# Performance work log

Measured on AMD Instinct MI355X. Metric: run time of the kernel, lower is better.

The kernel has to match this reference:

```python
import jax, jax.numpy as jnp
import numpy as np

WIN = 8          # window size
P = 32           # patch grid side (patch_w_num)
SHIFTS = (0, 4)  # stride=[0,4] -> regular + shifted window branches
HEADS = 16
DH = 64          # dim_head
DIM = 512
HP = HEADS // len(SHIFTS)   # heads per shift branch
NW = (P // WIN) ** 2        # windows per image (16)
WS = WIN * WIN              # tokens per window (64)


def _rel_index():
    c = np.stack(np.meshgrid(np.arange(WIN), np.arange(WIN), indexing="ij")).reshape(2, -1)
    r = (c[:, :, None] - c[:, None, :]).transpose(1, 2, 0) + WIN - 1
    return (r[..., 0] * (2 * WIN - 1) + r[..., 1]).astype(np.int32)  # [WS, WS]

REL_IDX = _rel_index()


def _shift_mask(shift):
    # standard Swin attention mask for cyclic shift
    img = np.zeros((P, P), np.int32); cnt = 0
    sl = (slice(0, -WIN), slice(-WIN, -shift), slice(-shift, None))
    for hs in sl:
        for ws_ in sl:
            img[hs, ws_] = cnt; cnt += 1
    m = img.reshape(P // WIN, WIN, P // WIN, WIN).transpose(0, 2, 1, 3).reshape(NW, WS)
    return np.where(m[:, None, :] != m[:, :, None], -1e9, 0.0).astype(np.float32)  # [NW, WS, WS]

MASK4 = _shift_mask(4)


def _part(t):
    # [B,P,P,hp,dh] -> [B*NW, hp, WS, dh]
    B, _, _, hp, dh = t.shape
    t = t.reshape(B, P // WIN, WIN, P // WIN, WIN, hp, dh)
    t = t.transpose(0, 1, 3, 2, 4, 5, 6).reshape(B * NW, WS, hp, dh)
    return t.transpose(0, 2, 1, 3)


def _merge(t, B):
    # [B*NW, hp, WS, dh] -> [B,P,P,hp,dh]
    hp, dh = t.shape[1], t.shape[3]
    t = t.transpose(0, 2, 1, 3).reshape(B, P // WIN, P // WIN, WIN, WIN, hp, dh)
    return t.transpose(0, 1, 3, 2, 4, 5, 6).reshape(B, P, P, hp, dh)


def setup_inputs() -> dict:
    key = jax.random.key(0)
    ks = jax.random.split(key, 5)
    B = 64
    x = jax.random.normal(ks[0], (B, P * P, DIM), jnp.float32)
    w_qkv = jax.random.normal(ks[1], (DIM, 3 * HEADS * DH), jnp.float32) * (DIM ** -0.5)
    bias_table = jax.random.normal(ks[2], ((2 * WIN - 1) ** 2, HEADS), jnp.float32) * 0.02
    w_out = jax.random.normal(ks[3], (HEADS * DH, DIM), jnp.float32) * ((HEADS * DH) ** -0.5)
    b_out = jnp.zeros((DIM,), jnp.float32)
    return {"x": x, "w_qkv": w_qkv, "bias_table": bias_table, "w_out": w_out, "b_out": b_out}


def reference(x, w_qkv, bias_table, w_out, b_out):
    B, N, _ = x.shape
    scale = DH ** -0.5
    qkv = (x @ w_qkv).reshape(B, P, P, 3, HEADS, DH)
    q, k, v = qkv[..., 0, :, :], qkv[..., 1, :, :], qkv[..., 2, :, :]  # [B,P,P,HEADS,DH]
    bias = bias_table[REL_IDX].transpose(2, 0, 1)  # [HEADS, WS, WS]
    mask4 = jnp.asarray(MASK4)
    outs = []
    for i, shift in enumerate(SHIFTS):
        hs = slice(i * HP, (i + 1) * HP)
        qi, ki, vi = q[..., hs, :], k[..., hs, :], v[..., hs, :]
        if shift:
            qi = jnp.roll(qi, (-shift, -shift), axis=(1, 2))
            ki = jnp.roll(ki, (-shift, -shift), axis=(1, 2))
            vi = jnp.roll(vi, (-shift, -shift), axis=(1, 2))
        qw, kw, vw = _part(qi), _part(ki), _part(vi)  # [B*NW, HP, WS, DH]
        attn = jnp.einsum("whid,whjd->whij", qw * scale, kw) + bias[hs][None]
        if shift:
            attn = attn.reshape(B, NW, HP, WS, WS) + mask4[None, :, None]
            attn = attn.reshape(B * NW, HP, WS, WS)
        attn = jax.nn.softmax(attn, axis=-1)
        ow = jnp.einsum("whij,whjd->whid", attn, vw)
        oi = _merge(ow, B)
        if shift:
            oi = jnp.roll(oi, (shift, shift), axis=(1, 2))
        outs.append(oi)
    out = jnp.concatenate(outs, axis=3).reshape(B, N, HEADS * DH)
    return out @ w_out + b_out
```

## Files before the change

### kernel.cpp

```cpp
#include <hip/hip_runtime.h>
#include <hip/hip_bf16.h>


typedef __attribute__((ext_vector_type(4))) float f32x4;
typedef __attribute__((ext_vector_type(8))) __bf16 bf16x8;
typedef __attribute__((ext_vector_type(8))) unsigned short u16x8;

__device__ __forceinline__ unsigned short f2bf(float f) {
  __hip_bfloat16 h = __float2bfloat16(f);
  return __builtin_bit_cast(unsigned short, h);
}
__device__ __forceinline__ float bf2f(unsigned short u) {
  return __builtin_bit_cast(float, ((unsigned int)u) << 16);
}

#define GLL16(gsrc, ldst)                                                              \
  __builtin_amdgcn_global_load_lds((const __attribute__((address_space(1))) void*)(gsrc), \
                                   (__attribute__((address_space(3))) void*)(ldst), 16, 0, 0)

#define SWZ(x) ((x) ^ ((((x) >> 7) & 3) << 4))

#define MFMA_BF16 __builtin_amdgcn_mfma_f32_16x16x32_bf16

__global__ __launch_bounds__(256) void cvt_x_kernel(const float* __restrict__ in,
                                                    unsigned short* __restrict__ out, int n4) {
  int i = blockIdx.x * blockDim.x + threadIdx.x;
  int stride = gridDim.x * blockDim.x;
  for (; i < n4; i += stride) {
    float4 v = reinterpret_cast<const float4*>(in)[i];
    ushort4 o;
    o.x = f2bf(v.x); o.y = f2bf(v.y); o.z = f2bf(v.z); o.w = f2bf(v.w);
    reinterpret_cast<ushort4*>(out)[i] = o;
  }
}

__global__ __launch_bounds__(256) void cvt_T_kernel(const float* __restrict__ in,
                                                    unsigned short* __restrict__ out,
                                                    int R, int C) {
  int idx = blockIdx.x * 256 + threadIdx.x;
  if (idx < R * C) {
    int r = idx / C, c = idx - r * C;
    out[(size_t)c * R + r] = f2bf(in[idx]);
  }
}

template <bool OUT_BF16>
__global__ __launch_bounds__(512, 4) void gemm2p(const unsigned short* __restrict__ A, int lda,
                                                 const unsigned short* __restrict__ B, int ldb,
                                                 void* __restrict__ Cv, int ldc,
                                                 const float* __restrict__ bias, int N, int K) {
  __shared__ alignas(16) unsigned char lds[49152];
  const int tid = threadIdx.x, lane = tid & 63, wave = tid >> 6;
  const int wm = wave >> 2, wn = wave & 3;
  const int nbn = N >> 8;
  const int nwg = gridDim.x;
  const int b0 = blockIdx.x;
  const int sb = (b0 & 7) * (nwg >> 3) + (b0 >> 3);
  const int bm = sb / nbn, bn = sb - bm * nbn;
  const int m0 = bm << 7, n0 = bn << 8;
  const int nkt = K >> 5;

  const int d0 = tid * 16;
  const int r0g = d0 >> 6;
  const int c0 = (SWZ(d0) & 63) >> 1;
  const int d1 = d0 + 8192;
  const int r1g = d1 >> 6;
  const int c1 = (SWZ(d1) & 63) >> 1;

  const int fr = lane & 15, fk = lane >> 4;
  const int fkb = fk * 16;

  auto STAGE_A = [&](const unsigned short* __restrict__ S, int ld, int kt, int base) {
    GLL16(S + (size_t)(m0 + r0g) * ld + kt * 32 + c0, &lds[base + wave * 1024]);
  };
  auto STAGE_B = [&](const unsigned short* __restrict__ S, int ld, int kt, int base) {
    auto* lb = &lds[base + wave * 1024];
    GLL16(S + (size_t)(n0 + r0g) * ld + kt * 32 + c0, lb);
    GLL16(S + (size_t)(n0 + r1g) * ld + kt * 32 + c1, lb + 8192);
  };
  auto LDA_ = [&](int abuf, int mi) -> bf16x8 {
    const int e = (wm * 64 + mi * 16 + fr) * 64 + fkb;
    return *reinterpret_cast<const bf16x8*>(&lds[abuf + SWZ(e)]);
  };
  auto LDB_ = [&](int bbuf, int ni) -> bf16x8 {
    const int e = (wn * 64 + ni * 16 + fr) * 64 + fkb;
    return *reinterpret_cast<const bf16x8*>(&lds[bbuf + SWZ(e)]);
  };

  STAGE_A(A, lda, 0, 0);
  STAGE_B(B, ldb, 0, 16384);
  STAGE_B(B, ldb, (nkt > 1) ? 1 : 0, 16384 + 16384);
  asm volatile("s_waitcnt vmcnt(2)" ::: "memory");
  __builtin_amdgcn_s_barrier();

  f32x4 acc[4][4] = {};
  bf16x8 Af[2], Bf[4];

  for (int u = 0; u < nkt; ++u) {
    const int abuf = (u & 1) * 8192;
    const int anx = ((u + 1) & 1) * 8192;
    const int bbuf = 16384 + (u & 1) * 16384;
    const int kA = (u + 1 < nkt) ? u + 1 : nkt - 1;
    const int kB = (u + 2 < nkt) ? u + 2 : nkt - 1;

    Af[0] = LDA_(abuf, 0);
    Af[1] = LDA_(abuf, 1);
#pragma unroll
    for (int ni = 0; ni < 4; ++ni) Bf[ni] = LDB_(bbuf, ni);
    STAGE_A(A, lda, kA, anx);
    __builtin_amdgcn_s_barrier();
    asm volatile("s_waitcnt lgkmcnt(0)" ::: "memory");
    __builtin_amdgcn_s_setprio(1);
#pragma unroll
    for (int mi = 0; mi < 2; ++mi)
#pragma unroll
      for (int ni = 0; ni < 4; ++ni)
        acc[mi][ni] = MFMA_BF16(Af[mi], Bf[ni], acc[mi][ni], 0, 0, 0);
    __builtin_amdgcn_s_setprio(0);
    __builtin_amdgcn_s_barrier();

    Af[0] = LDA_(abuf, 2);
    Af[1] = LDA_(abuf, 3);
    STAGE_B(B, ldb, kB, bbuf);
    asm volatile("s_waitcnt vmcnt(2)" ::: "memory");
    __builtin_amdgcn_s_barrier();
    asm volatile("s_waitcnt lgkmcnt(0)" ::: "memory");
    __builtin_amdgcn_s_setprio(1);
#pragma unroll
    for (int mi = 0; mi < 2; ++mi)
#pragma unroll
      for (int ni = 0; ni < 4; ++ni)
        acc[2 + mi][ni] = MFMA_BF16(Af[mi], Bf[ni], acc[2 + mi][ni], 0, 0, 0);
    __builtin_amdgcn_s_setprio(0);
    __builtin_amdgcn_s_barrier();
  }

  const int er = fk << 2;
#pragma unroll
  for (int mi = 0; mi < 4; ++mi)
#pragma unroll
    for (int ni = 0; ni < 4; ++ni) {
      const int col = n0 + wn * 64 + ni * 16 + fr;
#pragma unroll
      for (int r = 0; r < 4; ++r) {
        const size_t row = (size_t)(m0 + wm * 64 + mi * 16 + er + r);
        if (OUT_BF16)
          ((unsigned short*)Cv)[row * ldc + col] = f2bf(acc[mi][ni][r]);
        else
          ((float*)Cv)[row * ldc + col] = acc[mi][ni][r] + bias[col];
      }
    }
}

__device__ __forceinline__ int region_of(int wy, int wx, int t) {
  int yr = wy * 8 + (t >> 3);
  int xr = wx * 8 + (t & 7);
  int ry = (yr < 24) ? 0 : ((yr < 28) ? 1 : 2);
  int rx = (xr < 24) ? 0 : ((xr < 28) ? 1 : 2);
  return ry * 3 + rx;
}

__global__ __launch_bounds__(256) void win_attn(const unsigned short* __restrict__ qkv,
                                                const float* __restrict__ bias_table,
                                                unsigned short* __restrict__ out,
                                                int nb16) {
  __shared__ alignas(16) unsigned short vt[4][64][72];
  __shared__ alignas(16) unsigned short pl[4][64][72];
  __shared__ unsigned short bias_sh[225 * 16];

  const int tid = threadIdx.x, lane = tid & 63, wave = tid >> 6;
  const int bid = blockIdx.x;
  const int g = bid / nb16;
  const int bw = bid - g * nb16;
  const int b = bw >> 4, w = bw & 15;
  const int wy = w >> 2, wx = w & 3;
  const int shift = g ? 4 : 0;

  for (int i = tid; i < 225 * 16; i += 256) bias_sh[i] = f2bf(bias_table[i]);
  __syncthreads();

  const int r0 = lane & 15, hi4 = lane >> 4;

  for (int hh = 0; hh < 2; ++hh) {
    const int head = g * 8 + wave * 2 + hh;
    const int qcol = head * 64;

    bf16x8 qf[4][2], kf[4][2];
#pragma unroll
    for (int mi = 0; mi < 4; ++mi) {
      const int t = mi * 16 + r0;
      const int y = (wy * 8 + (t >> 3) + shift) & 31;
      const int x = (wx * 8 + (t & 7) + shift) & 31;
      const size_t base = (size_t)((b << 10) + (y << 5) + x) * 3072 + qcol;
#pragma unroll
      for (int kb = 0; kb < 2; ++kb) {
        const int d = kb * 32 + hi4 * 8;
        qf[mi][kb] = *reinterpret_cast<const bf16x8*>(&qkv[base + d]);
        kf[mi][kb] = *reinterpret_cast<const bf16x8*>(&qkv[base + 1024 + d]);
      }
    }

    {
      const int y = (wy * 8 + (lane >> 3) + shift) & 31;
      const int x = (wx * 8 + (lane & 7) + shift) & 31;
      const unsigned short* vsrc =
          qkv + (size_t)((b << 10) + (y << 5) + x) * 3072 + 2048 + qcol;
#pragma unroll
      for (int d0 = 0; d0 < 8; ++d0) {
        u16x8 vv = *reinterpret_cast<const u16x8*>(&vsrc[d0 * 8]);
#pragma unroll
        for (int jj = 0; jj < 8; ++jj) vt[wave][d0 * 8 + jj][lane] = vv[jj];
      }
    }

    f32x4 s[4][4] = {};
#pragma unroll
    for (int mi = 0; mi < 4; ++mi)
#pragma unroll
      for (int ni = 0; ni < 4; ++ni) {
        s[mi][ni] = MFMA_BF16(qf[mi][0], kf[ni][0], s[mi][ni], 0, 0, 0);
        s[mi][ni] = MFMA_BF16(qf[mi][1], kf[ni][1], s[mi][ni], 0, 0, 0);
      }

    int rj[4];
#pragma unroll
    for (int ni = 0; ni < 4; ++ni) rj[ni] = region_of(wy, wx, ni * 16 + r0);
    float rinv[4][4];
#pragma unroll
    for (int mi = 0; mi < 4; ++mi) {
#pragma unroll
      for (int r = 0; r < 4; ++r) {
        const int it = mi * 16 + hi4 * 4 + r;
        const int iy = it >> 3, ix = it & 7;
        const int ri = region_of(wy, wx, it);
        float vals[4], vmax = -1e30f;
#pragma unroll
        for (int ni = 0; ni < 4; ++ni) {
          const int jt = ni * 16 + r0;
          const int ridx = (iy - (jt >> 3) + 7) * 15 + (ix - (jt & 7) + 7);
          float v = s[mi][ni][r] * 0.125f + bf2f(bias_sh[ridx * 16 + head]);
          if (g && ri != rj[ni]) v = -1e9f;
          vals[ni] = v;
          vmax = fmaxf(vmax, v);
        }
        vmax = fmaxf(vmax, __shfl_xor(vmax, 1));
        vmax = fmaxf(vmax, __shfl_xor(vmax, 2));
        vmax = fmaxf(vmax, __shfl_xor(vmax, 4));
        vmax = fmaxf(vmax, __shfl_xor(vmax, 8));
        float ssum = 0.f;
#pragma unroll
        for (int ni = 0; ni < 4; ++ni) {
          float p = __expf(vals[ni] - vmax);
          ssum += p;
          s[mi][ni][r] = p;
        }
        ssum += __shfl_xor(ssum, 1);
        ssum += __shfl_xor(ssum, 2);
        ssum += __shfl_xor(ssum, 4);
        ssum += __shfl_xor(ssum, 8);
        rinv[mi][r] = 1.0f / ssum;
      }
    }

#pragma unroll
    for (int mi = 0; mi < 4; ++mi)
#pragma unroll
      for (int ni = 0; ni < 4; ++ni)
#pragma unroll
        for (int r = 0; r < 4; ++r)
          pl[wave][mi * 16 + hi4 * 4 + r][ni * 16 + r0] = f2bf(s[mi][ni][r]);

    f32x4 o[4][4] = {};
#pragma unroll
    for (int kb = 0; kb < 2; ++kb) {
      bf16x8 pf[4], vf[4];
#pragma unroll
      for (int mi = 0; mi < 4; ++mi)
        pf[mi] = *reinterpret_cast<const bf16x8*>(&pl[wave][mi * 16 + r0][kb * 32 + hi4 * 8]);
#pragma unroll
      for (int di = 0; di < 4; ++di)
        vf[di] = *reinterpret_cast<const bf16x8*>(&vt[wave][di * 16 + r0][kb * 32 + hi4 * 8]);
#pragma unroll
      for (int mi = 0; mi < 4; ++mi)
#pragma unroll
        for (int di = 0; di < 4; ++di)
          o[mi][di] = MFMA_BF16(pf[mi], vf[di], o[mi][di], 0, 0, 0);
    }

#pragma unroll
    for (int mi = 0; mi < 4; ++mi)
#pragma unroll
      for (int r = 0; r < 4; ++r) {
        const int it = mi * 16 + hi4 * 4 + r;
        const int y = (wy * 8 + (it >> 3) + shift) & 31;
        const int x = (wx * 8 + (it & 7) + shift) & 31;
        unsigned short* op = out + (size_t)((b << 10) + (y << 5) + x) * 3072 + head * 64;
        const float rv = rinv[mi][r];
#pragma unroll
        for (int di = 0; di < 4; ++di) op[di * 16 + r0] = f2bf(o[mi][di][r] * rv);
      }
  }
}

extern "C" void kernel_launch(void* const* d_in, const int* in_sizes, int n_in,
                              void* d_out, int out_size, void* d_ws, size_t ws_size,
                              hipStream_t stream) {
  const float* x = (const float*)d_in[0];
  const float* w_qkv = (const float*)d_in[1];
  const float* bias_table = (const float*)d_in[2];
  const float* w_out = (const float*)d_in[3];
  const float* b_out = (const float*)d_in[4];
  float* out = (float*)d_out;

  int S = 1;
  for (; S < 16; S <<= 1) {
    size_t need = 2ull * (2097152ull + 234881024ull / (size_t)S);
    if (need <= ws_size) break;
  }
  const int Mc = 65536 / S;
  const int nb = 64 / S;

  unsigned short* wqt = (unsigned short*)d_ws;
  unsigned short* wot = wqt + (size_t)1572864;
  unsigned short* xb  = wot + (size_t)524288;
  unsigned short* qkv = xb + (size_t)Mc * 512;

  cvt_T_kernel<<<6144, 256, 0, stream>>>(w_qkv, wqt, 512, 3072);
  cvt_T_kernel<<<2048, 256, 0, stream>>>(w_out, wot, 1024, 512);

  for (int c = 0; c < S; ++c) {
    const float* xc = x + (size_t)c * Mc * 512;
    cvt_x_kernel<<<2048, 256, 0, stream>>>(xc, xb, Mc * 128);
    gemm2p<true><<<(Mc >> 7) * 12, 512, 0, stream>>>(xb, 512, wqt, 512, (void*)qkv, 3072,
                                                     nullptr, 3072, 512);
    win_attn<<<2 * nb * 16, 256, 0, stream>>>(qkv, bias_table, qkv, nb * 16);
    gemm2p<false><<<(Mc >> 7) * 2, 512, 0, stream>>>(qkv, 3072, wot, 1024,
                                                     (void*)(out + (size_t)c * Mc * 512), 512,
                                                     b_out, 512, 1024);
  }
}
```

Baseline: 602.3 us.

## Triple-buffer GEMM LDS staging with one barrier per k-step

Replaces the GEMM's split A/B double-buffer schedule, which had four barriers per k-step, with a three-stage ring buffer. Each k-step issues a combined A+B prefetch two steps ahead and ends with a single vmcnt wait and barrier. The goal is to cut barrier and synchronisation overhead and hide global-load latency better. The cost is raising LDS use from 48KB to 72KB per block, which may lower the number of resident blocks per CU.

```diff
diff --git a/kernel.cpp b/kernel.cpp
--- a/kernel.cpp
+++ b/kernel.cpp
@@ -45,11 +45,11 @@
 }
 
 template <bool OUT_BF16>
-__global__ __launch_bounds__(512, 4) void gemm2p(const unsigned short* __restrict__ A, int lda,
+__global__ __launch_bounds__(512, 4) void gemm3d(const unsigned short* __restrict__ A, int lda,
                                                  const unsigned short* __restrict__ B, int ldb,
                                                  void* __restrict__ Cv, int ldc,
                                                  const float* __restrict__ bias, int N, int K) {
-  __shared__ alignas(16) unsigned char lds[49152];
+  __shared__ alignas(16) unsigned char lds[73728];
   const int tid = threadIdx.x, lane = tid & 63, wave = tid >> 6;
   const int wm = wave >> 2, wn = wave & 3;
   const int nbn = N >> 8;
@@ -70,46 +70,42 @@
   const int fr = lane & 15, fk = lane >> 4;
   const int fkb = fk * 16;
 
-  auto STAGE_A = [&](const unsigned short* __restrict__ S, int ld, int kt, int base) {
-    GLL16(S + (size_t)(m0 + r0g) * ld + kt * 32 + c0, &lds[base + wave * 1024]);
+  auto STAGE = [&](int kt, int buf) {
+    const int ab = buf * 24576;
+    GLL16(A + (size_t)(m0 + r0g) * lda + kt * 32 + c0, &lds[ab + wave * 1024]);
+    auto* lb = &lds[ab + 8192 + wave * 1024];
+    GLL16(B + (size_t)(n0 + r0g) * ldb + kt * 32 + c0, lb);
+    GLL16(B + (size_t)(n0 + r1g) * ldb + kt * 32 + c1, lb + 8192);
   };
-  auto STAGE_B = [&](const unsigned short* __restrict__ S, int ld, int kt, int base) {
-    auto* lb = &lds[base + wave * 1024];
-    GLL16(S + (size_t)(n0 + r0g) * ld + kt * 32 + c0, lb);
-    GLL16(S + (size_t)(n0 + r1g) * ld + kt * 32 + c1, lb + 8192);
+  auto LDA_ = [&](int buf, int mi) -> bf16x8 {
+    const int e = (wm * 64 + mi * 16 + fr) * 64 + fkb;
+    return *reinterpret_cast<const bf16x8*>(&lds[buf * 24576 + SWZ(e)]);
   };
-  auto LDA_ = [&](int abuf, int mi) -> bf16x8 {
-    const int e = (wm * 64 + mi * 16 + fr) * 64 + fkb;
-    return *reinterpret_cast<const bf16x8*>(&lds[abuf + SWZ(e)]);
+  auto LDB_ = [&](int buf, int ni) -> bf16x8 {
+    const int e = (wn * 64 + ni * 16 + fr) * 64 + fkb;
+    return *reinterpret_cast<const bf16x8*>(&lds[buf * 24576 + 8192 + SWZ(e)]);
   };
-  auto LDB_ = [&](int bbuf, int ni) -> bf16x8 {
-    const int e = (wn * 64 + ni * 16 + fr) * 64 + fkb;
-    return *reinterpret_cast<const bf16x8*>(&lds[bbuf + SWZ(e)]);
-  };
-
-  STAGE_A(A, lda, 0, 0);
-  STAGE_B(B, ldb, 0, 16384);
-  STAGE_B(B, ldb, (nkt > 1) ? 1 : 0, 16384 + 16384);
-  asm volatile("s_waitcnt vmcnt(2)" ::: "memory");
+
+  STAGE(0, 0);
+  STAGE((nkt > 1) ? 1 : 0, 1);
+  asm volatile("s_waitcnt vmcnt(3)" ::: "memory");
   __builtin_amdgcn_s_barrier();
+  __builtin_amdgcn_sched_barrier(0);
 
   f32x4 acc[4][4] = {};
   bf16x8 Af[2], Bf[4];
 
   for (int u = 0; u < nkt; ++u) {
-    const int abuf = (u & 1) * 8192;
-    const int anx = ((u + 1) & 1) * 8192;
-    const int bbuf = 16384 + (u & 1) * 16384;
-    const int kA = (u + 1 < nkt) ? u + 1 : nkt - 1;
-    const int kB = (u + 2 < nkt) ? u + 2 : nkt - 1;
-
-    Af[0] = LDA_(abuf, 0);
-    Af[1] = LDA_(abuf, 1);
-#pragma unroll
-    for (int ni = 0; ni < 4; ++ni) Bf[ni] = LDB_(bbuf, ni);
-    STAGE_A(A, lda, kA, anx);
-    __builtin_amdgcn_s_barrier();
-    asm volatile("s_waitcnt lgkmcnt(0)" ::: "memory");
+    const int cb = u % 3;
+    const int sbuf = (u + 2) % 3;
+    const int kS = (u + 2 < nkt) ? u + 2 : nkt - 1;
+
+    STAGE(kS, sbuf);
+
+    Af[0] = LDA_(cb, 0);
+    Af[1] = LDA_(cb, 1);
+#pragma unroll
+    for (int ni = 0; ni < 4; ++ni) Bf[ni] = LDB_(cb, ni);
     __builtin_amdgcn_s_setprio(1);
 #pragma unroll
     for (int mi = 0; mi < 2; ++mi)
@@ -117,14 +113,8 @@
       for (int ni = 0; ni < 4; ++ni)
         acc[mi][ni] = MFMA_BF16(Af[mi], Bf[ni], acc[mi][ni], 0, 0, 0);
     __builtin_amdgcn_s_setprio(0);
-    __builtin_amdgcn_s_barrier();
-
-    Af[0] = LDA_(abuf, 2);
-    Af[1] = LDA_(abuf, 3);
-    STAGE_B(B, ldb, kB, bbuf);
-    asm volatile("s_waitcnt vmcnt(2)" ::: "memory");
-    __builtin_amdgcn_s_barrier();
-    asm volatile("s_waitcnt lgkmcnt(0)" ::: "memory");
+    Af[0] = LDA_(cb, 2);
+    Af[1] = LDA_(cb, 3);
     __builtin_amdgcn_s_setprio(1);
 #pragma unroll
     for (int mi = 0; mi < 2; ++mi)
@@ -132,7 +122,10 @@
       for (int ni = 0; ni < 4; ++ni)
         acc[2 + mi][ni] = MFMA_BF16(Af[mi], Bf[ni], acc[2 + mi][ni], 0, 0, 0);
     __builtin_amdgcn_s_setprio(0);
+
+    asm volatile("s_waitcnt vmcnt(3)" ::: "memory");
     __builtin_amdgcn_s_barrier();
+    __builtin_amdgcn_sched_barrier(0);
   }
 
   const int er = fk << 2;
@@ -331,10 +324,10 @@
   for (int c = 0; c < S; ++c) {
     const float* xc = x + (size_t)c * Mc * 512;
     cvt_x_kernel<<<2048, 256, 0, stream>>>(xc, xb, Mc * 128);
-    gemm2p<true><<<(Mc >> 7) * 12, 512, 0, stream>>>(xb, 512, wqt, 512, (void*)qkv, 3072,
+    gemm3d<true><<<(Mc >> 7) * 12, 512, 0, stream>>>(xb, 512, wqt, 512, (void*)qkv, 3072,
                                                      nullptr, 3072, 512);
     win_attn<<<2 * nb * 16, 256, 0, stream>>>(qkv, bias_table, qkv, nb * 16);
-    gemm2p<false><<<(Mc >> 7) * 2, 512, 0, stream>>>(qkv, 3072, wot, 1024,
+    gemm3d<false><<<(Mc >> 7) * 2, 512, 0, stream>>>(qkv, 3072, wot, 1024,
                                                      (void*)(out + (size_t)c * Mc * 512), 512,
                                                      b_out, 512, 1024);
   }
```

Measured after the change: 615.7 us. 2.2% more time.
